# Optimization experiments

Hardware: AMD Instinct MI355X
Metric: run time of the kernel (lower is better)

## Reference

```python
import jax, jax.numpy as jnp
import numpy as np

INPUT_DIM, HIDDEN, NUM_CLASSES = 16, 128, 24
B, T = 4096, 1024  # raw I/Q frame (B, 2, T); seq_len = 2*T/INPUT_DIM = 128


def setup_inputs() -> dict:
    key = jax.random.key(0)
    ks = jax.random.split(key, 12)
    s = 1.0 / np.sqrt(HIDDEN)  # torch default uniform bound ~ use scaled normal
    def w(k, shape, scale):
        return jax.random.normal(k, shape, jnp.float32) * scale
    return {
        "x": jax.random.normal(ks[0], (B, 2, T), jnp.float32),
        "w_ih1": w(ks[1], (3 * HIDDEN, INPUT_DIM), s),
        "w_hh1": w(ks[2], (3 * HIDDEN, HIDDEN), s),
        "b_ih1": w(ks[3], (3 * HIDDEN,), s),
        "b_hh1": w(ks[4], (3 * HIDDEN,), s),
        "w_ih2": w(ks[5], (3 * HIDDEN, HIDDEN), s),
        "w_hh2": w(ks[6], (3 * HIDDEN, HIDDEN), s),
        "b_ih2": w(ks[7], (3 * HIDDEN,), s),
        "b_hh2": w(ks[8], (3 * HIDDEN,), s),
        "fc_w": w(ks[9], (NUM_CLASSES, HIDDEN), s),
        "fc_b": w(ks[10], (NUM_CLASSES,), s),
    }


def _gru_layer(x, w_ih, w_hh, b_ih, b_hh, return_seq=True):
    # x: (B, L, D). PyTorch GRU gate order: r, z, n.
    Bb = x.shape[0]
    H = w_hh.shape[1]
    xp = jnp.einsum('bld,gd->blg', x, w_ih) + b_ih  # (B, L, 3H) precomputed input proj

    def step(h, xt):
        gh = h @ w_hh.T + b_hh  # (B, 3H)
        ir, iz, inn = jnp.split(xt, 3, axis=-1)
        hr, hz, hn = jnp.split(gh, 3, axis=-1)
        r = jax.nn.sigmoid(ir + hr)
        z = jax.nn.sigmoid(iz + hz)
        n = jnp.tanh(inn + r * hn)
        h_new = (1.0 - z) * n + z * h
        return h_new, (h_new if return_seq else 0.0)

    h0 = jnp.zeros((Bb, H), x.dtype)
    h_last, ys = jax.lax.scan(step, h0, jnp.swapaxes(xp, 0, 1))
    if return_seq:
        return jnp.swapaxes(ys, 0, 1)
    return h_last


def reference(x, w_ih1, w_hh1, b_ih1, b_hh1, w_ih2, w_hh2, b_ih2, b_hh2, fc_w, fc_b):
    Bb = x.shape[0]
    # (B,2,T) -> (B,2,L,8) -> (B,L,2,8) -> (B,L,16)
    h = x.reshape(Bb, 2, -1, INPUT_DIM // 2)
    h = jnp.swapaxes(h, 1, 2).reshape(Bb, -1, INPUT_DIM)
    seq1 = _gru_layer(h, w_ih1, w_hh1, b_ih1, b_hh1, return_seq=True)
    last = _gru_layer(seq1, w_ih2, w_hh2, b_ih2, b_hh2, return_seq=False)
    return last @ fc_w.T + fc_b
```

## Files before the change

### kernel.cpp

```cpp
#include <hip/hip_runtime.h>


typedef _Float16 half_t;
typedef _Float16 half8 __attribute__((ext_vector_type(8)));
typedef _Float16 half4v __attribute__((ext_vector_type(4)));
typedef float f32x4 __attribute__((ext_vector_type(4)));

#define BB 16
#define HS 136
#define XS 520

#define NL2E (-1.442695041f)
#define L2E2 (2.885390082f)

static __device__ __forceinline__ f32x4 mfma16(half8 a, half8 b, f32x4 c) {
  return __builtin_amdgcn_mfma_f32_16x16x32_f16(a, b, c, 0, 0, 0);
}

static __device__ __forceinline__ void pin(half8& v) {
  f32x4 t = __builtin_bit_cast(f32x4, v);
  asm volatile("" : "+v"(t));
  v = __builtin_bit_cast(half8, t);
}

static __device__ __forceinline__ half8 zero8() {
  half8 v;
#pragma unroll
  for (int i = 0; i < 8; ++i) v[i] = (half_t)0.f;
  return v;
}

static __device__ __forceinline__ half8 ldw8s(const float* __restrict__ p, float s) {
  float4 a = *(const float4*)p;
  float4 b = *(const float4*)(p + 4);
  half8 r;
  r[0] = (half_t)(a.x * s); r[1] = (half_t)(a.y * s);
  r[2] = (half_t)(a.z * s); r[3] = (half_t)(a.w * s);
  r[4] = (half_t)(b.x * s); r[5] = (half_t)(b.y * s);
  r[6] = (half_t)(b.z * s); r[7] = (half_t)(b.w * s);
  return r;
}

static __device__ __forceinline__ float ex2(float x) { return __builtin_amdgcn_exp2f(x); }
static __device__ __forceinline__ float rcpa(float x) { return __builtin_amdgcn_rcpf(x); }

__global__ __launch_bounds__(512, 2) void gru_fused(
    const float* __restrict__ x,
    const float* __restrict__ wih1, const float* __restrict__ whh1,
    const float* __restrict__ bih1, const float* __restrict__ bhh1,
    const float* __restrict__ wih2, const float* __restrict__ whh2,
    const float* __restrict__ bih2, const float* __restrict__ bhh2,
    const float* __restrict__ fcw, const float* __restrict__ fcb,
    float* __restrict__ out)
{
  __shared__ __align__(16) half_t xl[BB][XS];
  __shared__ __align__(16) half_t h1b[2][BB][HS];
  __shared__ __align__(16) half_t h2b[2][BB][HS];
  __shared__ float h2f[BB][129];

  const int tid = threadIdx.x;
  const int lane = tid & 63;
  const int wv = tid >> 6;
  const int q = lane >> 4;
  const int c = lane & 15;
  const int jc = wv * 16 + c;
  const int s0 = blockIdx.x * BB;

  for (int i = tid; i < 2 * BB * HS; i += 512) {
    ((half_t*)h1b)[i] = (half_t)0.f;
    ((half_t*)h2b)[i] = (half_t)0.f;
  }

  const float eb1r = ex2(NL2E * (bih1[jc] + bhh1[jc]));
  const float eb1z = ex2(NL2E * (bih1[128 + jc] + bhh1[128 + jc]));
  const float b1in = L2E2 * bih1[256 + jc];
  const float b1hn = L2E2 * bhh1[256 + jc];
  const float eb2r = ex2(NL2E * (bih2[jc] + bhh2[jc]));
  const float eb2z = ex2(NL2E * (bih2[128 + jc] + bhh2[128 + jc]));
  const float b2in = L2E2 * bih2[256 + jc];
  const float b2hn = L2E2 * bhh2[256 + jc];

  half8 wi1r, wi1z, wi1n;
  if (q < 2) {
    wi1r = ldw8s(wih1 + (0 * 128 + jc) * 16 + q * 8, NL2E);
    wi1z = ldw8s(wih1 + (1 * 128 + jc) * 16 + q * 8, NL2E);
    wi1n = ldw8s(wih1 + (2 * 128 + jc) * 16 + q * 8, L2E2);
  } else {
    wi1r = zero8(); wi1z = zero8(); wi1n = zero8();
  }
  pin(wi1r); pin(wi1z); pin(wi1n);

  half8 wh1r[4], wh1z[4], wh1n[4], wi2r[4], wi2z[4], wi2n[4], wh2r[4], wh2z[4], wh2n[4];
#pragma unroll
  for (int kk = 0; kk < 4; ++kk) {
    const int ko = kk * 32 + q * 8;
    wh1r[kk] = ldw8s(whh1 + (0 * 128 + jc) * 128 + ko, NL2E);
    wh1z[kk] = ldw8s(whh1 + (1 * 128 + jc) * 128 + ko, NL2E);
    wh1n[kk] = ldw8s(whh1 + (2 * 128 + jc) * 128 + ko, L2E2);
    wi2r[kk] = ldw8s(wih2 + (0 * 128 + jc) * 128 + ko, NL2E);
    wi2z[kk] = ldw8s(wih2 + (1 * 128 + jc) * 128 + ko, NL2E);
    wi2n[kk] = ldw8s(wih2 + (2 * 128 + jc) * 128 + ko, L2E2);
    wh2r[kk] = ldw8s(whh2 + (0 * 128 + jc) * 128 + ko, NL2E);
    wh2z[kk] = ldw8s(whh2 + (1 * 128 + jc) * 128 + ko, NL2E);
    wh2n[kk] = ldw8s(whh2 + (2 * 128 + jc) * 128 + ko, L2E2);
    pin(wh1r[kk]); pin(wh1z[kk]); pin(wh1n[kk]);
    pin(wi2r[kk]); pin(wi2z[kk]); pin(wi2n[kk]);
    pin(wh2r[kk]); pin(wh2z[kk]); pin(wh2n[kk]);
  }

  float h1p[4] = {0.f, 0.f, 0.f, 0.f};
  float h2p[4] = {0.f, 0.f, 0.f, 0.f};

#pragma unroll 1
  for (int tc = 0; tc < 4; ++tc) {
#pragma unroll
    for (int it = 0; it < 4; ++it) {
      int idx = tid + it * 512;
      int s = idx >> 7;
      int rem = idx & 127;
      int ch = rem >> 6;
      int i4 = rem & 63;
      const float4 v = *(const float4*)(x + (size_t)(s0 + s) * 2048 + ch * 1024 + tc * 256 + i4 * 4);
      half4v hv;
      hv[0] = (half_t)v.x; hv[1] = (half_t)v.y; hv[2] = (half_t)v.z; hv[3] = (half_t)v.w;
      *(half4v*)&xl[s][(i4 >> 1) * 16 + ch * 8 + (i4 & 1) * 4] = hv;
    }
    __syncthreads();

#pragma unroll 2
    for (int tt = 0; tt < 32; ++tt) {
      const int i = tc * 32 + tt;
      const int rb = i & 1;
      const int wb = rb ^ 1;
      const float l2m = (i > 0) ? 1.f : 0.f;
      const f32x4 kZ = {0.f, 0.f, 0.f, 0.f};

      half8 ax = zero8();
      if (q < 2) ax = *(const half8*)&xl[c][tt * 16 + q * 8];
      half8 ah0 = *(const half8*)&h1b[rb][c][q * 8];
      half8 a20 = *(const half8*)&h2b[rb][c][q * 8];

      f32x4 ar  = mfma16(ax, wi1r, kZ);
      f32x4 az  = mfma16(ax, wi1z, kZ);
      f32x4 ain = mfma16(ax, wi1n, kZ);
      f32x4 ahn = mfma16(ah0, wh1n[0], kZ);
      ar = mfma16(ah0, wh1r[0], ar);
      az = mfma16(ah0, wh1z[0], az);
      f32x4 cr  = mfma16(ah0, wi2r[0], kZ);
      f32x4 cz  = mfma16(ah0, wi2z[0], kZ);
      f32x4 cin = mfma16(ah0, wi2n[0], kZ);
      f32x4 chn = mfma16(a20, wh2n[0], kZ);
      cr = mfma16(a20, wh2r[0], cr);
      cz = mfma16(a20, wh2z[0], cz);
#pragma unroll
      for (int kk = 1; kk < 4; ++kk) {
        half8 ah = *(const half8*)&h1b[rb][c][kk * 32 + q * 8];
        half8 a2 = *(const half8*)&h2b[rb][c][kk * 32 + q * 8];
        ar  = mfma16(ah, wh1r[kk], ar);
        az  = mfma16(ah, wh1z[kk], az);
        ahn = mfma16(ah, wh1n[kk], ahn);
        cr  = mfma16(ah, wi2r[kk], cr);
        cz  = mfma16(ah, wi2z[kk], cz);
        cin = mfma16(ah, wi2n[kk], cin);
        cr  = mfma16(a2, wh2r[kk], cr);
        cz  = mfma16(a2, wh2z[kk], cz);
        chn = mfma16(a2, wh2n[kk], chn);
      }

      float C1[4], rg1[4], zg1[4], C2[4], rg2[4], zg2[4];
#pragma unroll
      for (int r = 0; r < 4; ++r) {
        float er = ex2(ar[r]);
        float ez = ex2(az[r]);
        float A  = fmaf(er, eb1r, 1.f);
        float Bv = fmaf(ez, eb1z, 1.f);
        float R  = rcpa(A * Bv);
        rg1[r] = R * Bv; zg1[r] = R * A;
        float av = fmaf(rg1[r], ahn[r] + b1hn, ain[r] + b1in);
        C1[r] = 1.f + ex2(av);
      }
#pragma unroll
      for (int r = 0; r < 4; ++r) {
        float er = ex2(cr[r]);
        float ez = ex2(cz[r]);
        float A  = fmaf(er, eb2r, 1.f);
        float Bv = fmaf(ez, eb2z, 1.f);
        float R  = rcpa(A * Bv);
        rg2[r] = R * Bv; zg2[r] = R * A;
        float av = fmaf(rg2[r], chn[r] + b2hn, cin[r] + b2in);
        C2[r] = 1.f + ex2(av);
      }
#pragma unroll
      for (int p = 0; p < 4; p += 2) {
        float R1 = rcpa(C1[p] * C1[p + 1]);
        float n0 = fmaf(R1 * C1[p + 1], -2.f, 1.f);
        float n1 = fmaf(R1 * C1[p],     -2.f, 1.f);
        float e0 = fmaf(zg1[p],     h1p[p]     - n0, n0);
        float e1 = fmaf(zg1[p + 1], h1p[p + 1] - n1, n1);
        h1p[p] = e0; h1p[p + 1] = e1;
        h1b[wb][q * 4 + p][jc]     = (half_t)e0;
        h1b[wb][q * 4 + p + 1][jc] = (half_t)e1;
        float R2 = rcpa(C2[p] * C2[p + 1]);
        float m0 = fmaf(R2 * C2[p + 1], -2.f, 1.f);
        float m1 = fmaf(R2 * C2[p],     -2.f, 1.f);
        float g0 = fmaf(zg2[p],     h2p[p]     - m0, m0) * l2m;
        float g1 = fmaf(zg2[p + 1], h2p[p + 1] - m1, m1) * l2m;
        h2p[p] = g0; h2p[p + 1] = g1;
        h2b[wb][q * 4 + p][jc]     = (half_t)g0;
        h2b[wb][q * 4 + p + 1][jc] = (half_t)g1;
      }
      __syncthreads();
    }
  }

  {
    const f32x4 kZ = {0.f, 0.f, 0.f, 0.f};
    half8 a10 = *(const half8*)&h1b[0][c][q * 8];
    half8 a20 = *(const half8*)&h2b[0][c][q * 8];
    f32x4 cr  = mfma16(a10, wi2r[0], kZ);
    f32x4 cz  = mfma16(a10, wi2z[0], kZ);
    f32x4 cin = mfma16(a10, wi2n[0], kZ);
    f32x4 chn = mfma16(a20, wh2n[0], kZ);
    cr = mfma16(a20, wh2r[0], cr);
    cz = mfma16(a20, wh2z[0], cz);
#pragma unroll
    for (int kk = 1; kk < 4; ++kk) {
      half8 a1 = *(const half8*)&h1b[0][c][kk * 32 + q * 8];
      half8 a2 = *(const half8*)&h2b[0][c][kk * 32 + q * 8];
      cr  = mfma16(a1, wi2r[kk], cr);
      cz  = mfma16(a1, wi2z[kk], cz);
      cin = mfma16(a1, wi2n[kk], cin);
      cr  = mfma16(a2, wh2r[kk], cr);
      cz  = mfma16(a2, wh2z[kk], cz);
      chn = mfma16(a2, wh2n[kk], chn);
    }
    float C2[4], rg2[4], zg2[4];
#pragma unroll
    for (int r = 0; r < 4; ++r) {
      float er = ex2(cr[r]);
      float ez = ex2(cz[r]);
      float A  = fmaf(er, eb2r, 1.f);
      float Bv = fmaf(ez, eb2z, 1.f);
      float R  = rcpa(A * Bv);
      rg2[r] = R * Bv; zg2[r] = R * A;
      float av = fmaf(rg2[r], chn[r] + b2hn, cin[r] + b2in);
      C2[r] = 1.f + ex2(av);
    }
#pragma unroll
    for (int p = 0; p < 4; p += 2) {
      float R2 = rcpa(C2[p] * C2[p + 1]);
      float m0 = fmaf(R2 * C2[p + 1], -2.f, 1.f);
      float m1 = fmaf(R2 * C2[p],     -2.f, 1.f);
      h2p[p]     = fmaf(zg2[p],     h2p[p]     - m0, m0);
      h2p[p + 1] = fmaf(zg2[p + 1], h2p[p + 1] - m1, m1);
    }
  }

#pragma unroll
  for (int r = 0; r < 4; ++r) h2f[q * 4 + r][jc] = h2p[r];
  __syncthreads();
  if (tid < 384) {
    const int m = tid & 15;
    const int cls = tid >> 4;
    const float* w = fcw + cls * 128;
    float acc = fcb[cls];
#pragma unroll 8
    for (int j = 0; j < 128; ++j) acc = fmaf(h2f[m][j], w[j], acc);
    out[(size_t)(s0 + m) * 24 + cls] = acc;
  }
}

extern "C" void kernel_launch(void* const* d_in, const int* in_sizes, int n_in,
                              void* d_out, int out_size, void* d_ws, size_t ws_size,
                              hipStream_t stream) {
  (void)in_sizes; (void)n_in; (void)d_ws; (void)ws_size; (void)out_size;
  const float* x    = (const float*)d_in[0];
  const float* wih1 = (const float*)d_in[1];
  const float* whh1 = (const float*)d_in[2];
  const float* bih1 = (const float*)d_in[3];
  const float* bhh1 = (const float*)d_in[4];
  const float* wih2 = (const float*)d_in[5];
  const float* whh2 = (const float*)d_in[6];
  const float* bih2 = (const float*)d_in[7];
  const float* bhh2 = (const float*)d_in[8];
  const float* fcw  = (const float*)d_in[9];
  const float* fcb  = (const float*)d_in[10];
  float* outp = (float*)d_out;
  gru_fused<<<dim3(256), dim3(512), 0, stream>>>(
      x, wih1, whh1, bih1, bhh1, wih2, whh2, bih2, bhh2, fcw, fcb, outp);
}
```

Measured before the change: 261.7 us.

## Double-buffer input chunks with register prefetch and pack gate math into float2 vectors

The input tile buffer is doubled so the next 256-sample chunk of x is loaded into registers at the start of each chunk and written to the alternate LDS buffer after the 32 recurrent steps. This hides global-load latency behind the recurrence instead of stalling at each chunk boundary. Separately, the GRU gate nonlinearities are rewritten on float2 vectors so the compiler can emit packed FP32 ops (v_pk_fma/mul). The trade-off is more LDS (a second x buffer) and extra registers held for the prefetch across the inner loop, which could pressure occupancy at 512x2 launch bounds.

Result: slower. 269.7 us (+3.0%).

```diff
diff --git a/kernel.cpp b/kernel.cpp
--- a/kernel.cpp
+++ b/kernel.cpp
@@ -5,6 +5,7 @@
 typedef _Float16 half8 __attribute__((ext_vector_type(8)));
 typedef _Float16 half4v __attribute__((ext_vector_type(4)));
 typedef float f32x4 __attribute__((ext_vector_type(4)));
+typedef float f32x2 __attribute__((ext_vector_type(2)));
 
 #define BB 16
 #define HS 136
@@ -43,6 +44,33 @@
 
 static __device__ __forceinline__ float ex2(float x) { return __builtin_amdgcn_exp2f(x); }
 static __device__ __forceinline__ float rcpa(float x) { return __builtin_amdgcn_rcpf(x); }
+static __device__ __forceinline__ f32x2 splat2(float s) {
+  f32x2 v; v[0] = s; v[1] = s; return v;
+}
+
+static __device__ __forceinline__ f32x2 gate_pair(
+    float arp0, float arp1, float azp0, float azp1,
+    float ahnp0, float ahnp1, float ainp0, float ainp1,
+    f32x2 ebr2, f32x2 ebz2, f32x2 bhn2, f32x2 bin2, f32x2 hp) {
+  const f32x2 one2 = splat2(1.f);
+  f32x2 er; er[0] = ex2(arp0); er[1] = ex2(arp1);
+  f32x2 ez; ez[0] = ex2(azp0); ez[1] = ex2(azp1);
+  f32x2 A  = er * ebr2 + one2;
+  f32x2 Bv = ez * ebz2 + one2;
+  f32x2 P  = A * Bv;
+  f32x2 R; R[0] = rcpa(P[0]); R[1] = rcpa(P[1]);
+  f32x2 rg = R * Bv;
+  f32x2 zg = R * A;
+  f32x2 hn; hn[0] = ahnp0; hn[1] = ahnp1; hn += bhn2;
+  f32x2 inn; inn[0] = ainp0; inn[1] = ainp1; inn += bin2;
+  f32x2 av = rg * hn + inn;
+  f32x2 C; C[0] = 1.f + ex2(av[0]); C[1] = 1.f + ex2(av[1]);
+  float RT = rcpa(C[0] * C[1]);
+  f32x2 Cs; Cs[0] = C[1]; Cs[1] = C[0];
+  f32x2 n = (splat2(RT) * Cs) * splat2(-2.f) + one2;
+  f32x2 d = hp - n;
+  return zg * d + n;
+}
 
 __global__ __launch_bounds__(512, 2) void gru_fused(
     const float* __restrict__ x,
@@ -53,7 +81,7 @@
     const float* __restrict__ fcw, const float* __restrict__ fcb,
     float* __restrict__ out)
 {
-  __shared__ __align__(16) half_t xl[BB][XS];
+  __shared__ __align__(16) half_t xl[2][BB][XS];
   __shared__ __align__(16) half_t h1b[2][BB][HS];
   __shared__ __align__(16) half_t h2b[2][BB][HS];
   __shared__ float h2f[BB][129];
@@ -71,14 +99,24 @@
     ((half_t*)h2b)[i] = (half_t)0.f;
   }
 
-  const float eb1r = ex2(NL2E * (bih1[jc] + bhh1[jc]));
-  const float eb1z = ex2(NL2E * (bih1[128 + jc] + bhh1[128 + jc]));
-  const float b1in = L2E2 * bih1[256 + jc];
-  const float b1hn = L2E2 * bhh1[256 + jc];
-  const float eb2r = ex2(NL2E * (bih2[jc] + bhh2[jc]));
-  const float eb2z = ex2(NL2E * (bih2[128 + jc] + bhh2[128 + jc]));
-  const float b2in = L2E2 * bih2[256 + jc];
-  const float b2hn = L2E2 * bhh2[256 + jc];
+  int st_s[4], st_ch[4], st_i4[4];
+#pragma unroll
+  for (int it = 0; it < 4; ++it) {
+    int idx = tid + it * 512;
+    st_s[it] = idx >> 7;
+    int rem = idx & 127;
+    st_ch[it] = rem >> 6;
+    st_i4[it] = rem & 63;
+  }
+
+  const f32x2 eb1r2 = splat2(ex2(NL2E * (bih1[jc] + bhh1[jc])));
+  const f32x2 eb1z2 = splat2(ex2(NL2E * (bih1[128 + jc] + bhh1[128 + jc])));
+  const f32x2 b1in2 = splat2(L2E2 * bih1[256 + jc]);
+  const f32x2 b1hn2 = splat2(L2E2 * bhh1[256 + jc]);
+  const f32x2 eb2r2 = splat2(ex2(NL2E * (bih2[jc] + bhh2[jc])));
+  const f32x2 eb2z2 = splat2(ex2(NL2E * (bih2[128 + jc] + bhh2[128 + jc])));
+  const f32x2 b2in2 = splat2(L2E2 * bih2[256 + jc]);
+  const f32x2 b2hn2 = splat2(L2E2 * bhh2[256 + jc]);
 
   half8 wi1r, wi1z, wi1n;
   if (q < 2) {
@@ -108,35 +146,41 @@
     pin(wh2r[kk]); pin(wh2z[kk]); pin(wh2n[kk]);
   }
 
-  float h1p[4] = {0.f, 0.f, 0.f, 0.f};
-  float h2p[4] = {0.f, 0.f, 0.f, 0.f};
+  f32x2 h1p2[2], h2p2[2];
+  h1p2[0] = splat2(0.f); h1p2[1] = splat2(0.f);
+  h2p2[0] = splat2(0.f); h2p2[1] = splat2(0.f);
+
+#pragma unroll
+  for (int it = 0; it < 4; ++it) {
+    const float4 v = *(const float4*)(x + (size_t)(s0 + st_s[it]) * 2048 +
+                                      st_ch[it] * 1024 + 0 * 256 + st_i4[it] * 4);
+    half4v hv;
+    hv[0] = (half_t)v.x; hv[1] = (half_t)v.y; hv[2] = (half_t)v.z; hv[3] = (half_t)v.w;
+    *(half4v*)&xl[0][st_s[it]][(st_i4[it] >> 1) * 16 + st_ch[it] * 8 + (st_i4[it] & 1) * 4] = hv;
+  }
+  __syncthreads();
 
 #pragma unroll 1
   for (int tc = 0; tc < 4; ++tc) {
-#pragma unroll
-    for (int it = 0; it < 4; ++it) {
-      int idx = tid + it * 512;
-      int s = idx >> 7;
-      int rem = idx & 127;
-      int ch = rem >> 6;
-      int i4 = rem & 63;
-      const float4 v = *(const float4*)(x + (size_t)(s0 + s) * 2048 + ch * 1024 + tc * 256 + i4 * 4);
-      half4v hv;
-      hv[0] = (half_t)v.x; hv[1] = (half_t)v.y; hv[2] = (half_t)v.z; hv[3] = (half_t)v.w;
-      *(half4v*)&xl[s][(i4 >> 1) * 16 + ch * 8 + (i4 & 1) * 4] = hv;
-    }
-    __syncthreads();
+    const int cb = tc & 1;
+    float4 pf[4];
+    if (tc < 3) {
+#pragma unroll
+      for (int it = 0; it < 4; ++it)
+        pf[it] = *(const float4*)(x + (size_t)(s0 + st_s[it]) * 2048 +
+                                  st_ch[it] * 1024 + (tc + 1) * 256 + st_i4[it] * 4);
+    }
 
 #pragma unroll 2
     for (int tt = 0; tt < 32; ++tt) {
       const int i = tc * 32 + tt;
       const int rb = i & 1;
       const int wb = rb ^ 1;
-      const float l2m = (i > 0) ? 1.f : 0.f;
+      const f32x2 l2m2 = splat2((i > 0) ? 1.f : 0.f);
       const f32x4 kZ = {0.f, 0.f, 0.f, 0.f};
 
       half8 ax = zero8();
-      if (q < 2) ax = *(const half8*)&xl[c][tt * 16 + q * 8];
+      if (q < 2) ax = *(const half8*)&xl[cb][c][tt * 16 + q * 8];
       half8 ah0 = *(const half8*)&h1b[rb][c][q * 8];
       half8 a20 = *(const half8*)&h2b[rb][c][q * 8];
 
@@ -167,47 +211,34 @@
         chn = mfma16(a2, wh2n[kk], chn);
       }
 
-      float C1[4], rg1[4], zg1[4], C2[4], rg2[4], zg2[4];
-#pragma unroll
-      for (int r = 0; r < 4; ++r) {
-        float er = ex2(ar[r]);
-        float ez = ex2(az[r]);
-        float A  = fmaf(er, eb1r, 1.f);
-        float Bv = fmaf(ez, eb1z, 1.f);
-        float R  = rcpa(A * Bv);
-        rg1[r] = R * Bv; zg1[r] = R * A;
-        float av = fmaf(rg1[r], ahn[r] + b1hn, ain[r] + b1in);
-        C1[r] = 1.f + ex2(av);
+#pragma unroll
+      for (int e = 0; e < 2; ++e) {
+        const int p = 2 * e;
+        f32x2 h1n = gate_pair(ar[p], ar[p + 1], az[p], az[p + 1],
+                              ahn[p], ahn[p + 1], ain[p], ain[p + 1],
+                              eb1r2, eb1z2, b1hn2, b1in2, h1p2[e]);
+        h1p2[e] = h1n;
+        h1b[wb][q * 4 + p][jc]     = (half_t)h1n[0];
+        h1b[wb][q * 4 + p + 1][jc] = (half_t)h1n[1];
+        f32x2 h2n = gate_pair(cr[p], cr[p + 1], cz[p], cz[p + 1],
+                              chn[p], chn[p + 1], cin[p], cin[p + 1],
+                              eb2r2, eb2z2, b2hn2, b2in2, h2p2[e]);
+        h2n *= l2m2;
+        h2p2[e] = h2n;
+        h2b[wb][q * 4 + p][jc]     = (half_t)h2n[0];
+        h2b[wb][q * 4 + p + 1][jc] = (half_t)h2n[1];
       }
-#pragma unroll
-      for (int r = 0; r < 4; ++r) {
-        float er = ex2(cr[r]);
-        float ez = ex2(cz[r]);
-        float A  = fmaf(er, eb2r, 1.f);
-        float Bv = fmaf(ez, eb2z, 1.f);
-        float R  = rcpa(A * Bv);
-        rg2[r] = R * Bv; zg2[r] = R * A;
-        float av = fmaf(rg2[r], chn[r] + b2hn, cin[r] + b2in);
-        C2[r] = 1.f + ex2(av);
-      }
-#pragma unroll
-      for (int p = 0; p < 4; p += 2) {
-        float R1 = rcpa(C1[p] * C1[p + 1]);
-        float n0 = fmaf(R1 * C1[p + 1], -2.f, 1.f);
-        float n1 = fmaf(R1 * C1[p],     -2.f, 1.f);
-        float e0 = fmaf(zg1[p],     h1p[p]     - n0, n0);
-        float e1 = fmaf(zg1[p + 1], h1p[p + 1] - n1, n1);
-        h1p[p] = e0; h1p[p + 1] = e1;
-        h1b[wb][q * 4 + p][jc]     = (half_t)e0;
-        h1b[wb][q * 4 + p + 1][jc] = (half_t)e1;
-        float R2 = rcpa(C2[p] * C2[p + 1]);
-        float m0 = fmaf(R2 * C2[p + 1], -2.f, 1.f);
-        float m1 = fmaf(R2 * C2[p],     -2.f, 1.f);
-        float g0 = fmaf(zg2[p],     h2p[p]     - m0, m0) * l2m;
-        float g1 = fmaf(zg2[p + 1], h2p[p + 1] - m1, m1) * l2m;
-        h2p[p] = g0; h2p[p + 1] = g1;
-        h2b[wb][q * 4 + p][jc]     = (half_t)g0;
-        h2b[wb][q * 4 + p + 1][jc] = (half_t)g1;
+      __syncthreads();
+    }
+
+    if (tc < 3) {
+#pragma unroll
+      for (int it = 0; it < 4; ++it) {
+        half4v hv;
+        hv[0] = (half_t)pf[it].x; hv[1] = (half_t)pf[it].y;
+        hv[2] = (half_t)pf[it].z; hv[3] = (half_t)pf[it].w;
+        *(half4v*)&xl[cb ^ 1][st_s[it]][(st_i4[it] >> 1) * 16 + st_ch[it] * 8 +
+                                        (st_i4[it] & 1) * 4] = hv;
       }
       __syncthreads();
     }
@@ -234,30 +265,20 @@
       cz  = mfma16(a2, wh2z[kk], cz);
       chn = mfma16(a2, wh2n[kk], chn);
     }
-    float C2[4], rg2[4], zg2[4];
-#pragma unroll
-    for (int r = 0; r < 4; ++r) {
-      float er = ex2(cr[r]);
-      float ez = ex2(cz[r]);
-      float A  = fmaf(er, eb2r, 1.f);
-      float Bv = fmaf(ez, eb2z, 1.f);
-      float R  = rcpa(A * Bv);
-      rg2[r] = R * Bv; zg2[r] = R * A;
-      float av = fmaf(rg2[r], chn[r] + b2hn, cin[r] + b2in);
-      C2[r] = 1.f + ex2(av);
-    }
-#pragma unroll
-    for (int p = 0; p < 4; p += 2) {
-      float R2 = rcpa(C2[p] * C2[p + 1]);
-      float m0 = fmaf(R2 * C2[p + 1], -2.f, 1.f);
-      float m1 = fmaf(R2 * C2[p],     -2.f, 1.f);
-      h2p[p]     = fmaf(zg2[p],     h2p[p]     - m0, m0);
-      h2p[p + 1] = fmaf(zg2[p + 1], h2p[p + 1] - m1, m1);
-    }
-  }
-
-#pragma unroll
-  for (int r = 0; r < 4; ++r) h2f[q * 4 + r][jc] = h2p[r];
+#pragma unroll
+    for (int e = 0; e < 2; ++e) {
+      const int p = 2 * e;
+      h2p2[e] = gate_pair(cr[p], cr[p + 1], cz[p], cz[p + 1],
+                          chn[p], chn[p + 1], cin[p], cin[p + 1],
+                          eb2r2, eb2z2, b2hn2, b2in2, h2p2[e]);
+    }
+  }
+
+#pragma unroll
+  for (int e = 0; e < 2; ++e) {
+    h2f[q * 4 + 2 * e][jc]     = h2p2[e][0];
+    h2f[q * 4 + 2 * e + 1][jc] = h2p2[e][1];
+  }
   __syncthreads();
   if (tid < 384) {
     const int m = tid & 15;
```
